# Kernel optimization log

Hardware: AMD Instinct MI355X
Metric: run time of the kernel (lower is better)

## Reference

```python
import jax, jax.numpy as jnp
import numpy as np

# MLA (multi-head latent attention) config
DIM = 1024
HEADS = 16
DIM_HEAD = DIM // HEADS          # 64
LATENT = DIM // 4                # 256, compressed KV latent dim
SCALE = DIM_HEAD ** -0.5


def setup_inputs() -> dict:
    key = jax.random.key(0)
    ks = jax.random.split(key, 8)
    B, S = 2, 2048
    init = lambda k, shape, fan_in: jax.random.normal(k, shape, jnp.float32) * (fan_in ** -0.5)
    return {
        "x":  jax.random.normal(ks[0], (B, S, DIM), jnp.float32),
        "Wq": init(ks[1], (DIM, DIM), DIM),
        "bq": jnp.zeros((DIM,), jnp.float32),
        "Wl": init(ks[2], (DIM, LATENT), DIM),      # down-projection to compressed KV latent
        "bl": jnp.zeros((LATENT,), jnp.float32),
        "Wk": init(ks[3], (LATENT, DIM), LATENT),   # latent -> per-head keys
        "bk": jnp.zeros((DIM,), jnp.float32),
        "Wv": init(ks[4], (LATENT, DIM), LATENT),   # latent -> per-head values
        "bv": jnp.zeros((DIM,), jnp.float32),
        "Wo": init(ks[5], (DIM, DIM), DIM),         # Attention.to_out
        "bo": jnp.zeros((DIM,), jnp.float32),
    }


def reference(x, Wq, bq, Wl, bl, Wk, bk, Wv, bv, Wo, bo):
    B, S, D = x.shape
    H, Dh = HEADS, DIM_HEAD
    # query projection
    q = (x @ Wq + bq).reshape(B, S, H, Dh)
    # compressed KV latent (this is what would be cached; kv_cache=None here)
    latent = x @ Wl + bl                              # [B, S, LATENT]
    k = (latent @ Wk + bk).reshape(B, S, H, Dh)
    v = (latent @ Wv + bv).reshape(B, S, H, Dh)
    # attention
    scores = jnp.einsum('bihd,bjhd->bhij', q, k) * SCALE   # [B, H, S, S]
    attn = jax.nn.softmax(scores, axis=-1)
    out = jnp.einsum('bhij,bjhd->bihd', attn, v).reshape(B, S, D)
    # dropout(p=0) is identity; output projection
    out = out @ Wo + bo
    return out
```

## Files before the change

kernel.cpp:

```cpp
#include <hip/hip_runtime.h>


typedef _Float16 half8  __attribute__((ext_vector_type(8)));
typedef _Float16 half4  __attribute__((ext_vector_type(4)));
typedef float    floatx4 __attribute__((ext_vector_type(4)));

__device__ __forceinline__ int swz_mask(int row) { return ((row ^ (row >> 2)) & 3) << 3; }

__global__ __launch_bounds__(256) void prep(
    const float* __restrict__ x,
    const float* __restrict__ Wq, const float* __restrict__ Wl,
    const float* __restrict__ Wk, const float* __restrict__ Wv,
    const float* __restrict__ Wo,
    _Float16* __restrict__ xh,
    _Float16* __restrict__ Bt1, _Float16* __restrict__ Bt2,
    _Float16* __restrict__ Wot)
{
    const int t = threadIdx.x;
    if (blockIdx.z == 5) {
        size_t gbase = ((size_t)(blockIdx.y * 32 + blockIdx.x) * 256 + t) * 16;
        const int row = (int)(gbase >> 10);
        const int m = swz_mask(row);
        const size_t rowbase = (size_t)row << 10;
        const int h0 = (int)(gbase & 1023);
#pragma unroll
        for (int it = 0; it < 4; ++it) {
            floatx4 v = *(const floatx4*)(x + gbase + it * 4);
            *(half4*)(xh + rowbase + ((h0 + it * 4) ^ m)) =
                __builtin_convertvector(v, half4);
        }
        return;
    }
    const float* src; _Float16* dst; int K, N;
    switch (blockIdx.z) {
        case 0:  src = Wq; dst = Bt1;                 K = 1024; N = 1024; break;
        case 1:  src = Wl; dst = Bt1 + 1024 * 1024;   K = 1024; N = 256;  break;
        case 2:  src = Wk; dst = Bt2;                 K = 256;  N = 1024; break;
        case 3:  src = Wv; dst = Bt2 + 1024 * 256;    K = 256;  N = 1024; break;
        default: src = Wo; dst = Wot;                 K = 1024; N = 1024; break;
    }
    const int n0 = blockIdx.x * 32, k0 = blockIdx.y * 32;
    if (n0 >= N || k0 >= K) return;
    __shared__ _Float16 tile[32][33];
    const int tx = t & 31, ty = t >> 5;
#pragma unroll
    for (int i = 0; i < 4; ++i)
        tile[ty + 8 * i][tx] = (_Float16)src[(size_t)(k0 + ty + 8 * i) * N + n0 + tx];
    __syncthreads();
#pragma unroll
    for (int i = 0; i < 4; ++i) {
        const int n = n0 + ty + 8 * i;
        dst[(size_t)n * K + ((k0 + tx) ^ swz_mask(n))] = tile[tx][ty + 8 * i];
    }
}

template <int MODE>
__global__ __launch_bounds__(256, 4) void gemm_fused(
    const _Float16* __restrict__ A, const _Float16* __restrict__ Bt,
    const float* __restrict__ bias0, const float* __restrict__ bias1,
    void* __restrict__ out0, void* __restrict__ out1,
    int N, int K)
{
    __shared__ _Float16 As[128 * 32];
    __shared__ _Float16 Bs[64 * 32];
    __shared__ _Float16 Tt[(MODE == 1) ? 64 * 136 : 1];
    const int t = threadIdx.x;
    const int lane = t & 63, w = t >> 6;
    const int quad = lane >> 4, low = lane & 15;
    const int row0 = blockIdx.y * 128, col0 = blockIdx.x * 64;
    const int wm = (w >> 1) * 64, wn = (w & 1) * 32;
    const int swz = ((low ^ (low >> 2)) & 3) << 3;

    floatx4 acc[4][2];
    const floatx4 z4 = {0.f, 0.f, 0.f, 0.f};
#pragma unroll
    for (int i = 0; i < 4; ++i)
#pragma unroll
        for (int j = 0; j < 2; ++j) acc[i][j] = z4;

    const int srow = lane >> 2;
    const int scol = (lane & 3) * 8;

    for (int k0 = 0; k0 < K; k0 += 32) {
        __syncthreads();
#pragma unroll
        for (int c = 0; c < 2; ++c) {
            const int chunk = w * 2 + c;
            const _Float16* g = A + (size_t)(row0 + chunk * 16 + srow) * K + k0 + scol;
            __builtin_amdgcn_global_load_lds(
                (const __attribute__((address_space(1))) void*)g,
                (__attribute__((address_space(3))) void*)(As + chunk * 512), 16, 0, 0);
        }
        {
            const _Float16* g = Bt + (size_t)(col0 + w * 16 + srow) * K + k0 + scol;
            __builtin_amdgcn_global_load_lds(
                (const __attribute__((address_space(1))) void*)g,
                (__attribute__((address_space(3))) void*)(Bs + w * 512), 16, 0, 0);
        }
        __syncthreads();

        half8 a[4], b[2];
#pragma unroll
        for (int i = 0; i < 4; ++i)
            a[i] = *(const half8*)(As + (wm + i * 16 + low) * 32 + ((quad * 8) ^ swz));
#pragma unroll
        for (int j = 0; j < 2; ++j)
            b[j] = *(const half8*)(Bs + (wn + j * 16 + low) * 32 + ((quad * 8) ^ swz));
#pragma unroll
        for (int i = 0; i < 4; ++i)
#pragma unroll
            for (int j = 0; j < 2; ++j)
                acc[i][j] = __builtin_amdgcn_mfma_f32_16x16x32_f16(a[i], b[j], acc[i][j], 0, 0, 0);
    }

    if (MODE == 1 && col0 >= 1024) {
        const int hh = (col0 - 1024) >> 6;
        const int bb = row0 >> 11;
        const int tok0 = row0 & 2047;
#pragma unroll
        for (int i = 0; i < 4; ++i)
#pragma unroll
            for (int j = 0; j < 2; ++j) {
                const int lc = wn + j * 16 + low;
                float bv = bias1[hh * 64 + lc];
                half4 ph;
#pragma unroll
                for (int r = 0; r < 4; ++r) ph[r] = (_Float16)(acc[i][j][r] + bv);
                *(half4*)(&Tt[lc * 136 + wm + i * 16 + quad * 4]) = ph;
            }
        __syncthreads();
        _Float16* vb = (_Float16*)out1 + ((size_t)(bb * 16 + hh) * 64) * 2048;
#pragma unroll
        for (int it = 0; it < 4; ++it) {
            const int e = t + 256 * it;
            const int d = e >> 4, tk = (e & 15) * 8;
            half8 val = *(const half8*)(&Tt[d * 136 + tk]);
            *(half8*)(vb + (size_t)d * 2048 + tok0 + tk) = val;
        }
        return;
    }

#pragma unroll
    for (int i = 0; i < 4; ++i) {
#pragma unroll
        for (int j = 0; j < 2; ++j) {
            const int col = col0 + wn + j * 16 + low;
            const int rbase = row0 + wm + i * 16 + quad * 4;
            if (MODE == 2) {
                const float bv = bias0[col];
#pragma unroll
                for (int r = 0; r < 4; ++r)
                    ((float*)out0)[(size_t)(rbase + r) * 1024 + col] = acc[i][j][r] + bv;
            } else if (col < 1024) {
                float bv = bias0[col];
#pragma unroll
                for (int r = 0; r < 4; ++r) {
                    float val = acc[i][j][r] + bv;
                    if (MODE == 0) val *= 0.125f;
                    ((_Float16*)out0)[(size_t)(rbase + r) * 1024 + col] = (_Float16)val;
                }
            } else {
                const int c2 = col - 1024;
                float bv = bias1[c2];
#pragma unroll
                for (int r = 0; r < 4; ++r) {
                    const int row = rbase + r;
                    ((_Float16*)out1)[(size_t)row * 256 + (c2 ^ swz_mask(row))] =
                        (_Float16)(acc[i][j][r] + bv);
                }
            }
        }
    }
}

__global__ __launch_bounds__(256, 2) void mla_attn(
    const _Float16* __restrict__ qp,
    const _Float16* __restrict__ kk,
    const _Float16* __restrict__ vt,
    _Float16* __restrict__ Op0, _Float16* __restrict__ Op1,
    float* __restrict__ lp)
{
    constexpr int S = 2048;
    __shared__ _Float16 Ks[64][76];
    __shared__ _Float16 Vs[64][76];
    __shared__ _Float16 Ps[256][76];

    const int t = threadIdx.x, lane = t & 63, w = t >> 6;
    const int quad = lane >> 4, low = lane & 15;
    const int q0 = blockIdx.x * 256;
    const int b = blockIdx.y >> 4, h = blockIdx.y & 15;
    const int split = blockIdx.z;

    half8 qf[4][2];
#pragma unroll
    for (int ni = 0; ni < 4; ++ni)
#pragma unroll
        for (int ks = 0; ks < 2; ++ks)
            qf[ni][ks] = *(const half8*)(qp +
                (size_t)(b * S + q0 + w * 64 + ni * 16 + low) * 1024 +
                h * 64 + ks * 32 + quad * 8);

    floatx4 oa[4][4], ls[4];
    const floatx4 z4 = {0.f, 0.f, 0.f, 0.f};
#pragma unroll
    for (int mi = 0; mi < 4; ++mi) {
        ls[mi] = z4;
#pragma unroll
        for (int nd = 0; nd < 4; ++nd) oa[mi][nd] = z4;
    }

    const _Float16* kbase = kk + (size_t)(b * S) * 1024 + h * 64;
    const _Float16* vbase = vt + (size_t)(b * 16 + h) * 64 * 2048;

    const int jbeg = split * 1024, jend = jbeg + 1024;
    for (int j0 = jbeg; j0 < jend; j0 += 64) {
        __syncthreads();
#pragma unroll
        for (int p = 0; p < 2; ++p) {
            int c = p * 256 + t;
            int r = c >> 3, o8 = (c & 7) * 8;
            *(half8*)(&Ks[r][o8]) = *(const half8*)(kbase + (size_t)(j0 + r) * 1024 + o8);
            *(half8*)(&Vs[r][o8]) = *(const half8*)(vbase + (size_t)r * 2048 + j0 + o8);
        }
        __syncthreads();

        floatx4 s[4][4];
        const floatx4 i4 = {-3.f, -3.f, -3.f, -3.f};
#pragma unroll
        for (int mj = 0; mj < 4; ++mj)
#pragma unroll
            for (int ni = 0; ni < 4; ++ni) s[mj][ni] = i4;
#pragma unroll
        for (int ks = 0; ks < 2; ++ks) {
            half8 af[4];
#pragma unroll
            for (int mj = 0; mj < 4; ++mj)
                af[mj] = *(const half8*)(&Ks[mj * 16 + low][ks * 32 + quad * 8]);
#pragma unroll
            for (int mj = 0; mj < 4; ++mj)
#pragma unroll
                for (int ni = 0; ni < 4; ++ni)
                    s[mj][ni] = __builtin_amdgcn_mfma_f32_16x16x32_f16(af[mj], qf[ni][ks], s[mj][ni], 0, 0, 0);
        }

#pragma unroll
        for (int mj = 0; mj < 4; ++mj)
#pragma unroll
            for (int ni = 0; ni < 4; ++ni) {
                floatx4 pv;
#pragma unroll
                for (int r = 0; r < 4; ++r) pv[r] = __expf(s[mj][ni][r]);
                ls[ni] += pv;
                half4 ph;
#pragma unroll
                for (int r = 0; r < 4; ++r) ph[r] = (_Float16)pv[r];
                *(half4*)(&Ps[w * 64 + ni * 16 + low][mj * 16 + quad * 4]) = ph;
            }

#pragma unroll
        for (int ks = 0; ks < 2; ++ks) {
            half8 pf[4], vf[4];
#pragma unroll
            for (int mi = 0; mi < 4; ++mi)
                pf[mi] = *(const half8*)(&Ps[w * 64 + mi * 16 + low][ks * 32 + quad * 8]);
#pragma unroll
            for (int nd = 0; nd < 4; ++nd)
                vf[nd] = *(const half8*)(&Vs[nd * 16 + low][ks * 32 + quad * 8]);
#pragma unroll
            for (int mi = 0; mi < 4; ++mi)
#pragma unroll
                for (int nd = 0; nd < 4; ++nd)
                    oa[mi][nd] = __builtin_amdgcn_mfma_f32_16x16x32_f16(pf[mi], vf[nd], oa[mi][nd], 0, 0, 0);
        }
    }

#pragma unroll
    for (int ni = 0; ni < 4; ++ni) {
        float l = ls[ni][0] + ls[ni][1] + ls[ni][2] + ls[ni][3];
        l += __shfl_xor(l, 16);
        l += __shfl_xor(l, 32);
        if (quad == 0)
            lp[split * 65536 + (b * 16 + h) * 2048 + q0 + w * 64 + ni * 16 + low] = l;
    }
    _Float16* op = split ? Op1 : Op0;
#pragma unroll
    for (int mi = 0; mi < 4; ++mi)
#pragma unroll
        for (int nd = 0; nd < 4; ++nd)
#pragma unroll
            for (int r = 0; r < 4; ++r)
                op[(size_t)(b * S + q0 + w * 64 + mi * 16 + quad * 4 + r) * 1024 +
                   h * 64 + nd * 16 + low] = (_Float16)oa[mi][nd][r];
}

__global__ __launch_bounds__(256) void attn_combine(
    const _Float16* __restrict__ O0, const _Float16* __restrict__ O1,
    const float* __restrict__ lp, _Float16* __restrict__ att)
{
    size_t idx = ((size_t)blockIdx.x * 256 + threadIdx.x) * 8;
    int row = (int)(idx >> 10), c = (int)(idx & 1023);
    int b = row >> 11, qq = row & 2047, h = c >> 6;
    int li = (b * 16 + h) * 2048 + qq;
    float inv = 1.f / (lp[li] + lp[65536 + li]);
    half8 a = *(const half8*)(O0 + idx);
    half8 bb = *(const half8*)(O1 + idx);
    half8 o;
#pragma unroll
    for (int r = 0; r < 8; ++r)
        o[r] = (_Float16)(((float)a[r] + (float)bb[r]) * inv);
    *(half8*)(att + ((size_t)row << 10) + (c ^ swz_mask(row))) = o;
}

extern "C" void kernel_launch(void* const* d_in, const int* in_sizes, int n_in,
                              void* d_out, int out_size, void* d_ws, size_t ws_size,
                              hipStream_t stream) {
    const float* x  = (const float*)d_in[0];
    const float* Wq = (const float*)d_in[1];
    const float* bq = (const float*)d_in[2];
    const float* Wl = (const float*)d_in[3];
    const float* bl = (const float*)d_in[4];
    const float* Wk = (const float*)d_in[5];
    const float* bk = (const float*)d_in[6];
    const float* Wv = (const float*)d_in[7];
    const float* bv = (const float*)d_in[8];
    const float* Wo = (const float*)d_in[9];
    const float* bo = (const float*)d_in[10];
    float* out = (float*)d_out;

    _Float16* p   = (_Float16*)d_ws;
    _Float16* xh  = p; p += 4194304;
    _Float16* qh  = p; p += 4194304;
    _Float16* kh  = p; p += 4194304;
    _Float16* vtb = p; p += 4194304;
    _Float16* ah  = p; p += 4194304;
    _Float16* lat = p; p += 1048576;
    _Float16* Bt1 = p; p += 1310720;
    _Float16* Bt2 = p; p += 524288;
    _Float16* Wot = p; p += 1048576;

    prep<<<dim3(32, 32, 6), 256, 0, stream>>>(x, Wq, Wl, Wk, Wv, Wo, xh, Bt1, Bt2, Wot);

    gemm_fused<0><<<dim3(20, 32), 256, 0, stream>>>(
        xh, Bt1, bq, bl, qh, lat, 1280, 1024);
    gemm_fused<1><<<dim3(32, 32), 256, 0, stream>>>(
        lat, Bt2, bk, bv, kh, vtb, 2048, 256);
    mla_attn<<<dim3(8, 32, 2), 256, 0, stream>>>(qh, kh, vtb, ah, xh, (float*)lat);
    attn_combine<<<2048, 256, 0, stream>>>(ah, xh, (const float*)lat, kh);
    gemm_fused<2><<<dim3(16, 32), 256, 0, stream>>>(
        kh, Wot, bo, nullptr, out, nullptr, 1024, 1024);
}
```

Baseline: 210.7 us.

## Double GEMM K-tile to 64 and move swizzle from stored layouts to load addressing

The GEMM now stages 64-wide K tiles in LDS instead of 32, halving the number of barrier-separated load phases and running two MFMA sub-steps per tile. The bank-conflict XOR swizzle is now applied when computing the global source address for the direct-to-LDS loads, so all producer kernels (prep, latent epilogue, combine) write plain row-major layouts. The occupancy hint in launch_bounds is dropped to accommodate the larger LDS footprint. The risks are lower occupancy from doubled shared memory and a mismatch if any consumer, such as the attention kernel, still expects the old swizzled layout.

```diff
diff --git a/kernel.cpp b/kernel.cpp
--- a/kernel.cpp
+++ b/kernel.cpp
@@ -4,8 +4,6 @@
 typedef _Float16 half8  __attribute__((ext_vector_type(8)));
 typedef _Float16 half4  __attribute__((ext_vector_type(4)));
 typedef float    floatx4 __attribute__((ext_vector_type(4)));
-
-__device__ __forceinline__ int swz_mask(int row) { return ((row ^ (row >> 2)) & 3) << 3; }
 
 __global__ __launch_bounds__(256) void prep(
     const float* __restrict__ x,
@@ -18,16 +16,11 @@
 {
     const int t = threadIdx.x;
     if (blockIdx.z == 5) {
-        size_t gbase = ((size_t)(blockIdx.y * 32 + blockIdx.x) * 256 + t) * 16;
-        const int row = (int)(gbase >> 10);
-        const int m = swz_mask(row);
-        const size_t rowbase = (size_t)row << 10;
-        const int h0 = (int)(gbase & 1023);
+        size_t base = ((size_t)(blockIdx.y * 32 + blockIdx.x) * 256 + t) * 16;
 #pragma unroll
         for (int it = 0; it < 4; ++it) {
-            floatx4 v = *(const floatx4*)(x + gbase + it * 4);
-            *(half4*)(xh + rowbase + ((h0 + it * 4) ^ m)) =
-                __builtin_convertvector(v, half4);
+            floatx4 v = *(const floatx4*)(x + base + it * 4);
+            *(half4*)(xh + base + it * 4) = __builtin_convertvector(v, half4);
         }
         return;
     }
@@ -48,28 +41,25 @@
         tile[ty + 8 * i][tx] = (_Float16)src[(size_t)(k0 + ty + 8 * i) * N + n0 + tx];
     __syncthreads();
 #pragma unroll
-    for (int i = 0; i < 4; ++i) {
-        const int n = n0 + ty + 8 * i;
-        dst[(size_t)n * K + ((k0 + tx) ^ swz_mask(n))] = tile[tx][ty + 8 * i];
-    }
+    for (int i = 0; i < 4; ++i)
+        dst[(size_t)(n0 + ty + 8 * i) * K + k0 + tx] = tile[tx][ty + 8 * i];
 }
 
 template <int MODE>
-__global__ __launch_bounds__(256, 4) void gemm_fused(
+__global__ __launch_bounds__(256) void gemm_fused(
     const _Float16* __restrict__ A, const _Float16* __restrict__ Bt,
     const float* __restrict__ bias0, const float* __restrict__ bias1,
     void* __restrict__ out0, void* __restrict__ out1,
     int N, int K)
 {
-    __shared__ _Float16 As[128 * 32];
-    __shared__ _Float16 Bs[64 * 32];
+    __shared__ _Float16 As[128 * 64];
+    __shared__ _Float16 Bs[64 * 64];
     __shared__ _Float16 Tt[(MODE == 1) ? 64 * 136 : 1];
     const int t = threadIdx.x;
     const int lane = t & 63, w = t >> 6;
     const int quad = lane >> 4, low = lane & 15;
     const int row0 = blockIdx.y * 128, col0 = blockIdx.x * 64;
     const int wm = (w >> 1) * 64, wn = (w & 1) * 32;
-    const int swz = ((low ^ (low >> 2)) & 3) << 3;
 
     floatx4 acc[4][2];
     const floatx4 z4 = {0.f, 0.f, 0.f, 0.f};
@@ -78,39 +68,50 @@
 #pragma unroll
         for (int j = 0; j < 2; ++j) acc[i][j] = z4;
 
-    const int srow = lane >> 2;
-    const int scol = (lane & 3) * 8;
-
-    for (int k0 = 0; k0 < K; k0 += 32) {
-        __syncthreads();
+    const int srow8 = lane >> 3;
+    const int sslot = lane & 7;
+    const int fswz = (low & 7);
+
+    for (int k0 = 0; k0 < K; k0 += 64) {
+        __syncthreads();
+#pragma unroll
+        for (int c = 0; c < 4; ++c) {
+            const int chunk = w * 4 + c;
+            const int row = chunk * 8 + srow8;
+            const int g = sslot ^ (row & 7);
+            const _Float16* gp = A + (size_t)(row0 + row) * K + k0 + g * 8;
+            __builtin_amdgcn_global_load_lds(
+                (const __attribute__((address_space(1))) void*)gp,
+                (__attribute__((address_space(3))) void*)(As + chunk * 512), 16, 0, 0);
+        }
 #pragma unroll
         for (int c = 0; c < 2; ++c) {
             const int chunk = w * 2 + c;
-            const _Float16* g = A + (size_t)(row0 + chunk * 16 + srow) * K + k0 + scol;
+            const int row = chunk * 8 + srow8;
+            const int g = sslot ^ (row & 7);
+            const _Float16* gp = Bt + (size_t)(col0 + row) * K + k0 + g * 8;
             __builtin_amdgcn_global_load_lds(
-                (const __attribute__((address_space(1))) void*)g,
-                (__attribute__((address_space(3))) void*)(As + chunk * 512), 16, 0, 0);
-        }
-        {
-            const _Float16* g = Bt + (size_t)(col0 + w * 16 + srow) * K + k0 + scol;
-            __builtin_amdgcn_global_load_lds(
-                (const __attribute__((address_space(1))) void*)g,
-                (__attribute__((address_space(3))) void*)(Bs + w * 512), 16, 0, 0);
-        }
-        __syncthreads();
-
-        half8 a[4], b[2];
-#pragma unroll
-        for (int i = 0; i < 4; ++i)
-            a[i] = *(const half8*)(As + (wm + i * 16 + low) * 32 + ((quad * 8) ^ swz));
-#pragma unroll
-        for (int j = 0; j < 2; ++j)
-            b[j] = *(const half8*)(Bs + (wn + j * 16 + low) * 32 + ((quad * 8) ^ swz));
-#pragma unroll
-        for (int i = 0; i < 4; ++i)
+                (const __attribute__((address_space(1))) void*)gp,
+                (__attribute__((address_space(3))) void*)(Bs + chunk * 512), 16, 0, 0);
+        }
+        __syncthreads();
+
+#pragma unroll
+        for (int kk = 0; kk < 2; ++kk) {
+            const int slot = ((4 * kk + quad) ^ fswz) << 3;
+            half8 a[4], b[2];
+#pragma unroll
+            for (int i = 0; i < 4; ++i)
+                a[i] = *(const half8*)(As + (wm + i * 16 + low) * 64 + slot);
 #pragma unroll
             for (int j = 0; j < 2; ++j)
-                acc[i][j] = __builtin_amdgcn_mfma_f32_16x16x32_f16(a[i], b[j], acc[i][j], 0, 0, 0);
+                b[j] = *(const half8*)(Bs + (wn + j * 16 + low) * 64 + slot);
+#pragma unroll
+            for (int i = 0; i < 4; ++i)
+#pragma unroll
+                for (int j = 0; j < 2; ++j)
+                    acc[i][j] = __builtin_amdgcn_mfma_f32_16x16x32_f16(a[i], b[j], acc[i][j], 0, 0, 0);
+        }
     }
 
     if (MODE == 1 && col0 >= 1024) {
@@ -163,11 +164,9 @@
                 const int c2 = col - 1024;
                 float bv = bias1[c2];
 #pragma unroll
-                for (int r = 0; r < 4; ++r) {
-                    const int row = rbase + r;
-                    ((_Float16*)out1)[(size_t)row * 256 + (c2 ^ swz_mask(row))] =
+                for (int r = 0; r < 4; ++r)
+                    ((_Float16*)out1)[(size_t)(rbase + r) * 256 + c2] =
                         (_Float16)(acc[i][j][r] + bv);
-                }
             }
         }
     }
@@ -308,7 +307,7 @@
 #pragma unroll
     for (int r = 0; r < 8; ++r)
         o[r] = (_Float16)(((float)a[r] + (float)bb[r]) * inv);
-    *(half8*)(att + ((size_t)row << 10) + (c ^ swz_mask(row))) = o;
+    *(half8*)(att + idx) = o;
 }
 
 extern "C" void kernel_launch(void* const* d_in, const int* in_sizes, int n_in,
```

Result: no change. 206.6 us (-2.0%).
